# Kernel optimization log

Hardware: AMD Instinct MI355X
Metric: run time of the kernel (lower is better)

Reference implementation:

```python
import jax, jax.numpy as jnp
import numpy as np

N_NODES = 50000
N_EDGES = 400000
HEADS = 3
CH = 128
NEG_SLOPE = 0.2
EPS = 1e-16


def setup_inputs() -> dict:
    key = jax.random.key(0)
    ks = jax.random.split(key, 10)
    return {
        "x": jax.random.normal(ks[0], (N_NODES, 9), jnp.float32),
        "emb_w": jax.random.normal(ks[1], (9, 128), jnp.float32) * 0.1,
        "emb_b": jax.random.normal(ks[2], (128,), jnp.float32) * 0.1,
        "gat_w": jax.random.normal(ks[3], (128, HEADS * CH), jnp.float32) * 0.05,
        "att_src": jax.random.normal(ks[4], (HEADS, CH), jnp.float32) * 0.1,
        "att_dst": jax.random.normal(ks[5], (HEADS, CH), jnp.float32) * 0.1,
        "gat_bias": jax.random.normal(ks[6], (CH,), jnp.float32) * 0.1,
        "out_w": jax.random.normal(ks[7], (128, 4), jnp.float32) * 0.1,
        "out_b": jax.random.normal(ks[8], (4,), jnp.float32) * 0.1,
        "edge_index": jax.random.randint(ks[9], (2, N_EDGES), 0, N_NODES, jnp.int64 if jax.config.jax_enable_x64 else jnp.int32),
    }


def reference(x, emb_w, emb_b, gat_w, att_src, att_dst, gat_bias, out_w, out_b, edge_index):
    n = x.shape[0]
    h = x @ emb_w + emb_b                                   # [N,128]
    # add self loops (PyG GATConv default)
    loops = jnp.arange(n, dtype=edge_index.dtype)
    src = jnp.concatenate([edge_index[0], loops])
    dst = jnp.concatenate([edge_index[1], loops])
    xh = (h @ gat_w).reshape(n, HEADS, CH)                  # [N,H,C]
    a_src = jnp.einsum('nhc,hc->nh', xh, att_src)           # [N,H]
    a_dst = jnp.einsum('nhc,hc->nh', xh, att_dst)           # [N,H]
    e = a_src[src] + a_dst[dst]                             # [E,H]
    e = jax.nn.leaky_relu(e, NEG_SLOPE)
    # segment softmax over destination node
    e_max = jax.ops.segment_max(e, dst, num_segments=n)
    e = jnp.exp(e - e_max[dst])
    denom = jax.ops.segment_sum(e, dst, num_segments=n)
    alpha = e / (denom[dst] + EPS)                          # [E,H]
    msg = xh[src] * alpha[:, :, None]                       # [E,H,C]
    agg = jax.ops.segment_sum(msg, dst, num_segments=n)     # [N,H,C]
    out = agg.mean(axis=1) + gat_bias                       # concat=False -> head mean
    x_new = out + h                                         # residual
    return x_new @ out_w + out_b                            # [N,4]
```

## Files before the change

### kernel.cpp

```cpp
#include <hip/hip_runtime.h>
#include <hip/hip_bf16.h>
#include <cstdint>

#define NEG 0.2f
#define SBS 256
#define SCAN2_T 1024
#define PADK 56

typedef __attribute__((ext_vector_type(8))) short bf16x8;
typedef __attribute__((ext_vector_type(4))) float f32x4;

__device__ __forceinline__ float bf2f(unsigned short u){
  return __uint_as_float(((unsigned)u)<<16);
}
__device__ __forceinline__ unsigned short f2bf(float f){
  __hip_bfloat16 b = __float2bfloat16(f);
  return *reinterpret_cast<unsigned short*>(&b);
}

__global__ __launch_bounds__(256)
void prep_kernel(const float* __restrict__ gat_w, const float* __restrict__ att_src,
                 const float* __restrict__ att_dst, float* __restrict__ w_att_s,
                 float* __restrict__ w_att_d, unsigned short* __restrict__ Bt2)
{
  if (blockIdx.x < 192){
    int wave = threadIdx.x >> 6, lane = threadIdx.x & 63;
    int o = blockIdx.x*4 + wave;
    if (o >= 768) return;
    int isD = (o >= 384);
    int t = isD ? (o - 384) : o;
    int h = t >> 7, k = t & 127;
    const float* att = isD ? att_dst : att_src;
    int c = 2*lane;
    float g0 = gat_w[(size_t)k*384 + h*128 + c];
    float g1 = gat_w[(size_t)k*384 + h*128 + c + 1];
    float dot = g0*att[h*128+c] + g1*att[h*128+c+1];
    #pragma unroll
    for (int off=32; off; off>>=1) dot += __shfl_down(dot, off);
    if (lane==0){
      if (isD) w_att_d[t] = dot; else w_att_s[t] = dot;
    }
  } else {
    int i = (blockIdx.x-192)*256 + threadIdx.x;
    if (i >= 12*128*32) return;
    int ks  = i >> 12;
    int rem = i & 4095;
    int col = rem >> 5;
    int kk  = rem & 31;
    int t = ks*32 + kk;
    int h = t >> 7, k = t & 127;
    Bt2[i] = f2bf(gat_w[(size_t)k*384 + h*128 + col] * (1.f/3.f));
  }
}

__global__ __launch_bounds__(256)
void embed_kernel(const float* __restrict__ x, const float* __restrict__ emb_w,
                  const float* __restrict__ emb_b, const float* __restrict__ w_att_s,
                  const float* __restrict__ w_att_d,
                  unsigned short* __restrict__ h_bf, float* __restrict__ a_s,
                  float* __restrict__ a_d, int nN)
{
  int n = blockIdx.x*256 + threadIdx.x;
  if (n >= nN) return;

  float xv[9];
  #pragma unroll
  for (int k=0;k<9;k++) xv[k] = x[(size_t)n*9 + k];

  float s0=0.f,s1=0.f,s2=0.f, d0=0.f,d1=0.f,d2=0.f;
  unsigned short* hrow = h_bf + (size_t)n*128;

  #pragma unroll 4
  for (int c0=0; c0<128; c0+=8){
    unsigned short pk[8];
    #pragma unroll
    for (int j=0;j<8;j++){
      int c = c0 + j;
      float acc = emb_b[c];
      #pragma unroll
      for (int k=0;k<9;k++) acc += xv[k]*emb_w[k*128+c];
      pk[j] = f2bf(acc);
      s0 += acc*w_att_s[c]; s1 += acc*w_att_s[128+c]; s2 += acc*w_att_s[256+c];
      d0 += acc*w_att_d[c]; d1 += acc*w_att_d[128+c]; d2 += acc*w_att_d[256+c];
    }
    *(int4*)(hrow + c0) = *(int4*)pk;
  }
  a_s[(size_t)n*3+0]=s0; a_s[(size_t)n*3+1]=s1; a_s[(size_t)n*3+2]=s2;
  a_d[(size_t)n*3+0]=d0; a_d[(size_t)n*3+1]=d1; a_d[(size_t)n*3+2]=d2;
}

__global__ __launch_bounds__(256)
void deg_kernel(const int* __restrict__ ei, int* __restrict__ deg, int nE)
{
  int e = blockIdx.x*256 + threadIdx.x;
  if (e < nE) atomicAdd(&deg[ei[nE + e]], 1);
}

__global__ __launch_bounds__(SBS)
void blocksum_kernel(const int* __restrict__ deg, int* __restrict__ bsum, int nN)
{
  int i = blockIdx.x*SBS + threadIdx.x;
  int v = (i < nN) ? deg[i] : 0;
  #pragma unroll
  for (int off=32; off; off>>=1) v += __shfl_down(v, off);
  __shared__ int ws[SBS/64];
  if ((threadIdx.x&63)==0) ws[threadIdx.x>>6] = v;
  __syncthreads();
  if (threadIdx.x==0){
    int s=0;
    #pragma unroll
    for (int i2=0;i2<SBS/64;i2++) s += ws[i2];
    bsum[blockIdx.x]=s;
  }
}

__global__ __launch_bounds__(SCAN2_T)
void scansum_kernel(const int* __restrict__ bsum, int* __restrict__ boff, int nB)
{
  __shared__ int s[SCAN2_T];
  int t = threadIdx.x;
  int v = (t < nB) ? bsum[t] : 0;
  s[t] = v;
  __syncthreads();
  for (int off=1; off<SCAN2_T; off<<=1){
    int add = (t >= off) ? s[t-off] : 0;
    __syncthreads();
    s[t] += add;
    __syncthreads();
  }
  if (t < nB) boff[t] = (t==0) ? 0 : s[t-1];
}

__global__ __launch_bounds__(SBS)
void blockscan_kernel(const int* __restrict__ deg, const int* __restrict__ boff,
                      int* __restrict__ rowptr, int* __restrict__ cursor, int nN)
{
  __shared__ int s[SBS];
  int t = threadIdx.x;
  int i = blockIdx.x*SBS + t;
  int v = (i < nN) ? deg[i] : 0;
  s[t] = v;
  __syncthreads();
  for (int off=1; off<SBS; off<<=1){
    int add = (t >= off) ? s[t-off] : 0;
    __syncthreads();
    s[t] += add;
    __syncthreads();
  }
  int excl = boff[blockIdx.x] + ((t==0) ? 0 : s[t-1]);
  if (i < nN){ rowptr[i] = excl; cursor[i] = excl; }
  if (i == nN-1) rowptr[nN] = excl + v;
}

__global__ __launch_bounds__(256)
void scatter_kernel(const int* __restrict__ ei, int* __restrict__ cursor,
                    int* __restrict__ csr, int nE)
{
  int e = blockIdx.x*256 + threadIdx.x;
  if (e < nE){
    int s = ei[e], d = ei[nE + e];
    int pos = atomicAdd(&cursor[d], 1);
    csr[pos] = s;
  }
}

__global__ __launch_bounds__(256)
void gather_kernel(const int* __restrict__ rowptr, const int* __restrict__ csr,
                   const float* __restrict__ a_s, const float* __restrict__ a_d,
                   const unsigned short* __restrict__ h_bf,
                   unsigned short* __restrict__ hagg, int nN)
{
  int wave = threadIdx.x >> 6, lane = threadIdx.x & 63;
  int n = blockIdx.x*4 + wave;
  if (n >= nN) return;

  int ro  = rowptr[n];
  int deg = rowptr[n+1] - ro;
  int degT = deg + 1;
  float ad0 = a_d[(size_t)n*3+0], ad1 = a_d[(size_t)n*3+1], ad2 = a_d[(size_t)n*3+2];

  float d0=0.f, d1=0.f, d2=0.f;
  float acc00=0.f, acc01=0.f, acc10=0.f, acc11=0.f, acc20=0.f, acc21=0.f;

  for (int base=0; base<degT; base+=64){
    int i = base + lane;
    int sReg = n; float p0=0.f, p1=0.f, p2=0.f;
    if (i < degT){
      int s = (i < deg) ? csr[ro+i] : n;
      sReg = s;
      float e0 = a_s[(size_t)s*3+0] + ad0; e0 = e0>0.f ? e0 : NEG*e0;
      float e1 = a_s[(size_t)s*3+1] + ad1; e1 = e1>0.f ? e1 : NEG*e1;
      float e2 = a_s[(size_t)s*3+2] + ad2; e2 = e2>0.f ? e2 : NEG*e2;
      p0 = __expf(e0); p1 = __expf(e1); p2 = __expf(e2);
      d0 += p0; d1 += p1; d2 += p2;
    }
    int cnt = min(64, degT - base);
    for (int j=0;j<cnt;j++){
      int   s  = __shfl(sReg, j);
      float A0 = __shfl(p0, j);
      float A1 = __shfl(p1, j);
      float A2 = __shfl(p2, j);
      ushort2 hv = *(const ushort2*)(h_bf + (size_t)s*128 + 2*lane);
      float f0 = bf2f(hv.x), f1 = bf2f(hv.y);
      acc00 += A0*f0; acc01 += A0*f1;
      acc10 += A1*f0; acc11 += A1*f1;
      acc20 += A2*f0; acc21 += A2*f1;
    }
  }
  #pragma unroll
  for (int off=1; off<64; off<<=1){
    d0 += __shfl_xor(d0, off);
    d1 += __shfl_xor(d1, off);
    d2 += __shfl_xor(d2, off);
  }
  float w0 = 1.f/(d0+1e-16f);
  float w1 = 1.f/(d1+1e-16f);
  float w2 = 1.f/(d2+1e-16f);

  size_t base = (size_t)n*384 + 2*lane;
  ushort2 o0 = {f2bf(acc00*w0), f2bf(acc01*w0)};
  ushort2 o1 = {f2bf(acc10*w1), f2bf(acc11*w1)};
  ushort2 o2 = {f2bf(acc20*w2), f2bf(acc21*w2)};
  *(ushort2*)(hagg + base      ) = o0;
  *(ushort2*)(hagg + base + 128) = o1;
  *(ushort2*)(hagg + base + 256) = o2;
}

__global__ __launch_bounds__(256)
void gemm2_kernel(const unsigned short* __restrict__ hagg,
                  const unsigned short* __restrict__ Bt2,
                  const unsigned short* __restrict__ h_bf,
                  const float* __restrict__ gat_bias,
                  const float* __restrict__ out_w, const float* __restrict__ out_b,
                  float* __restrict__ out, int nN)
{
  __shared__ __align__(16) unsigned short Bs[2][128*PADK];
  int tid  = threadIdx.x;
  int wave = tid >> 6, lane = tid & 63;
  int cl = lane & 15, kg = lane >> 4;
  int r0 = blockIdx.x*64 + wave*16;
  int rowA = min(r0 + cl, nN-1);
  const unsigned short* aBase = hagg + (size_t)rowA*384 + kg*8;

  int scol = tid >> 1, shalf = tid & 1;
  int dstI = scol*(PADK/8) + shalf*2;

  {
    const int4* src = (const int4*)Bt2;
    int4 t0 = src[2*tid], t1 = src[2*tid+1];
    ((int4*)Bs[0])[dstI]   = t0;
    ((int4*)Bs[0])[dstI+1] = t1;
  }
  f32x4 acc[8];
  #pragma unroll
  for (int f=0;f<8;f++) acc[f] = (f32x4){0.f,0.f,0.f,0.f};
  bf16x8 aCur = *(const bf16x8*)(aBase);
  __syncthreads();

  #pragma unroll
  for (int ks=0; ks<12; ks++){
    int4 t0, t1; bf16x8 aNext;
    if (ks < 11){
      const int4* src = (const int4*)(Bt2 + (size_t)(ks+1)*4096);
      t0 = src[2*tid]; t1 = src[2*tid+1];
      aNext = *(const bf16x8*)(aBase + (ks+1)*32);
    }
    const unsigned short* bs = Bs[ks & 1];
    #pragma unroll
    for (int f=0;f<8;f++){
      bf16x8 b = *(const bf16x8*)(bs + (f*16 + cl)*PADK + kg*8);
      acc[f] = __builtin_amdgcn_mfma_f32_16x16x32_bf16(aCur, b, acc[f], 0, 0, 0);
    }
    if (ks < 11){
      int4* dst = (int4*)Bs[(ks+1) & 1];
      dst[dstI]   = t0;
      dst[dstI+1] = t1;
      aCur = aNext;
    }
    __syncthreads();
  }

  float p[4][4];
  #pragma unroll
  for (int r=0;r<4;r++)
    #pragma unroll
    for (int j=0;j<4;j++) p[r][j]=0.f;

  #pragma unroll
  for (int f=0;f<8;f++){
    int col = f*16 + cl;
    float bias = gat_bias[col];
    float w0=out_w[col*4+0], w1=out_w[col*4+1], w2=out_w[col*4+2], w3=out_w[col*4+3];
    #pragma unroll
    for (int r=0;r<4;r++){
      int row = r0 + kg*4 + r;
      float hres = (row < nN) ? bf2f(h_bf[(size_t)row*128 + col]) : 0.f;
      float xn = acc[f][r] + bias + hres;
      p[r][0] += xn*w0; p[r][1] += xn*w1; p[r][2] += xn*w2; p[r][3] += xn*w3;
    }
  }
  #pragma unroll
  for (int off=1; off<16; off<<=1){
    #pragma unroll
    for (int r=0;r<4;r++)
      #pragma unroll
      for (int j=0;j<4;j++) p[r][j] += __shfl_xor(p[r][j], off);
  }
  if (cl == 0){
    #pragma unroll
    for (int r=0;r<4;r++){
      int row = r0 + kg*4 + r;
      if (row < nN){
        float4 o = {p[r][0]+out_b[0], p[r][1]+out_b[1], p[r][2]+out_b[2], p[r][3]+out_b[3]};
        *(float4*)(out + (size_t)row*4) = o;
      }
    }
  }
}

extern "C" void kernel_launch(void* const* d_in, const int* in_sizes, int n_in,
                              void* d_out, int out_size, void* d_ws, size_t ws_size,
                              hipStream_t stream) {
  const float* x       = (const float*)d_in[0];
  const float* emb_w   = (const float*)d_in[1];
  const float* emb_b   = (const float*)d_in[2];
  const float* gat_w   = (const float*)d_in[3];
  const float* att_src = (const float*)d_in[4];
  const float* att_dst = (const float*)d_in[5];
  const float* gat_bias= (const float*)d_in[6];
  const float* out_w   = (const float*)d_in[7];
  const float* out_b   = (const float*)d_in[8];
  const int*   ei      = (const int*)d_in[9];
  float* out = (float*)d_out;

  int nN = in_sizes[0]/9;
  int nE = in_sizes[9]/2;
  int nB = (nN + SBS - 1) / SBS;

  char* p = (char*)d_ws;
  auto alloc = [&](size_t bytes)->char*{
    char* r = p; p += (bytes + 255) & ~(size_t)255; return r;
  };
  unsigned short* h_bf   = (unsigned short*)alloc((size_t)nN*128*2);
  float*          a_s    = (float*)         alloc((size_t)nN*3*4);
  float*          a_d    = (float*)         alloc((size_t)nN*3*4);
  float*          w_att_s= (float*)         alloc(384*4);
  float*          w_att_d= (float*)         alloc(384*4);
  unsigned short* Bt2    = (unsigned short*)alloc((size_t)12*128*32*2);
  int*            deg    = (int*)           alloc((size_t)nN*4);
  int*            rowptr = (int*)           alloc(((size_t)nN+1)*4);
  int*            cursor = (int*)           alloc((size_t)nN*4);
  int*            csr    = (int*)           alloc((size_t)nE*4);
  int*            bsum   = (int*)           alloc((size_t)nB*4);
  int*            boff   = (int*)           alloc((size_t)nB*4);
  unsigned short* hagg   = (unsigned short*)alloc((size_t)nN*384*2);

  hipMemsetAsync(deg, 0, (size_t)nN*4, stream);

  prep_kernel<<<384, 256, 0, stream>>>(gat_w, att_src, att_dst, w_att_s, w_att_d, Bt2);

  embed_kernel<<<(nN+255)/256, 256, 0, stream>>>(
      x, emb_w, emb_b, w_att_s, w_att_d, h_bf, a_s, a_d, nN);

  deg_kernel<<<(nE+255)/256, 256, 0, stream>>>(ei, deg, nE);
  blocksum_kernel<<<nB, SBS, 0, stream>>>(deg, bsum, nN);
  scansum_kernel<<<1, SCAN2_T, 0, stream>>>(bsum, boff, nB);
  blockscan_kernel<<<nB, SBS, 0, stream>>>(deg, boff, rowptr, cursor, nN);
  scatter_kernel<<<(nE+255)/256, 256, 0, stream>>>(ei, cursor, csr, nE);

  gather_kernel<<<(nN+3)/4, 256, 0, stream>>>(
      rowptr, csr, a_s, a_d, h_bf, hagg, nN);

  gemm2_kernel<<<(nN+63)/64, 256, 0, stream>>>(
      hagg, Bt2, h_bf, gat_bias, out_w, out_b, out, nN);
}
```

Baseline: 226.6 us.

## Process four destination nodes per wave with 16-lane groups and 16-byte gathers

The gather kernel now splits each wave into four 16-lane groups, one destination node per group. Each lane loads 8 bf16 features at once with a 16-byte vector load and handles two neighbours per inner iteration. Before, one wave per node did 4-byte loads and looped serially over every neighbour. The change is meant to cut idle lanes and per-edge shuffle overhead when average degree is about 9, and to widen memory transactions. In exchange it uses more registers (24 accumulators) and sees divergence when the nodes sharing a wave have different degrees.

```diff
diff --git a/kernel.cpp b/kernel.cpp
--- a/kernel.cpp
+++ b/kernel.cpp
@@ -8,6 +8,7 @@
 #define PADK 56
 
 typedef __attribute__((ext_vector_type(8))) short bf16x8;
+typedef __attribute__((ext_vector_type(8))) unsigned short ushort8;
 typedef __attribute__((ext_vector_type(4))) float f32x4;
 
 __device__ __forceinline__ float bf2f(unsigned short u){
@@ -171,22 +172,31 @@
                    unsigned short* __restrict__ hagg, int nN)
 {
   int wave = threadIdx.x >> 6, lane = threadIdx.x & 63;
-  int n = blockIdx.x*4 + wave;
-  if (n >= nN) return;
-
-  int ro  = rowptr[n];
-  int deg = rowptr[n+1] - ro;
-  int degT = deg + 1;
-  float ad0 = a_d[(size_t)n*3+0], ad1 = a_d[(size_t)n*3+1], ad2 = a_d[(size_t)n*3+2];
-
+  int g   = lane >> 4;
+  int lin = lane & 15;
+  int gb  = lane & 48;
+  int n = blockIdx.x*16 + wave*4 + g;
+  int valid = (n < nN);
+  int nc = valid ? n : (nN-1);
+
+  int ro  = rowptr[nc];
+  int deg = rowptr[nc+1] - ro;
+  int degT = valid ? (deg + 1) : 0;
+
+  float ad0 = a_d[(size_t)nc*3+0], ad1 = a_d[(size_t)nc*3+1], ad2 = a_d[(size_t)nc*3+2];
+
+  float acc0[8], acc1[8], acc2[8];
+  #pragma unroll
+  for (int c=0;c<8;c++){ acc0[c]=0.f; acc1[c]=0.f; acc2[c]=0.f; }
   float d0=0.f, d1=0.f, d2=0.f;
-  float acc00=0.f, acc01=0.f, acc10=0.f, acc11=0.f, acc20=0.f, acc21=0.f;
-
-  for (int base=0; base<degT; base+=64){
-    int i = base + lane;
-    int sReg = n; float p0=0.f, p1=0.f, p2=0.f;
+
+  const unsigned short* hb8 = h_bf + 8*lin;
+
+  for (int base=0; base<degT; base+=16){
+    int i = base + lin;
+    int sReg = nc; float p0=0.f, p1=0.f, p2=0.f;
     if (i < degT){
-      int s = (i < deg) ? csr[ro+i] : n;
+      int s = (i < deg) ? csr[ro+i] : nc;
       sReg = s;
       float e0 = a_s[(size_t)s*3+0] + ad0; e0 = e0>0.f ? e0 : NEG*e0;
       float e1 = a_s[(size_t)s*3+1] + ad1; e1 = e1>0.f ? e1 : NEG*e1;
@@ -194,36 +204,59 @@
       p0 = __expf(e0); p1 = __expf(e1); p2 = __expf(e2);
       d0 += p0; d1 += p1; d2 += p2;
     }
-    int cnt = min(64, degT - base);
-    for (int j=0;j<cnt;j++){
-      int   s  = __shfl(sReg, j);
-      float A0 = __shfl(p0, j);
-      float A1 = __shfl(p1, j);
-      float A2 = __shfl(p2, j);
-      ushort2 hv = *(const ushort2*)(h_bf + (size_t)s*128 + 2*lane);
-      float f0 = bf2f(hv.x), f1 = bf2f(hv.y);
-      acc00 += A0*f0; acc01 += A0*f1;
-      acc10 += A1*f0; acc11 += A1*f1;
-      acc20 += A2*f0; acc21 += A2*f1;
-    }
-  }
-  #pragma unroll
-  for (int off=1; off<64; off<<=1){
+    int cnt = min(16, degT - base);
+    int j = 0;
+    for (; j+1 < cnt; j += 2){
+      int   sA = __shfl(sReg, gb+j);
+      int   sB = __shfl(sReg, gb+j+1);
+      float A0 = __shfl(p0, gb+j),   A1 = __shfl(p1, gb+j),   A2 = __shfl(p2, gb+j);
+      float B0 = __shfl(p0, gb+j+1), B1 = __shfl(p1, gb+j+1), B2 = __shfl(p2, gb+j+1);
+      ushort8 ha = *(const ushort8*)(hb8 + (size_t)sA*128);
+      ushort8 hb = *(const ushort8*)(hb8 + (size_t)sB*128);
+      #pragma unroll
+      for (int c=0;c<8;c++){
+        float fa = bf2f(ha[c]);
+        float fb = bf2f(hb[c]);
+        acc0[c] += A0*fa + B0*fb;
+        acc1[c] += A1*fa + B1*fb;
+        acc2[c] += A2*fa + B2*fb;
+      }
+    }
+    if (j < cnt){
+      int   sA = __shfl(sReg, gb+j);
+      float A0 = __shfl(p0, gb+j), A1 = __shfl(p1, gb+j), A2 = __shfl(p2, gb+j);
+      ushort8 ha = *(const ushort8*)(hb8 + (size_t)sA*128);
+      #pragma unroll
+      for (int c=0;c<8;c++){
+        float fa = bf2f(ha[c]);
+        acc0[c] += A0*fa; acc1[c] += A1*fa; acc2[c] += A2*fa;
+      }
+    }
+  }
+
+  #pragma unroll
+  for (int off=1; off<16; off<<=1){
     d0 += __shfl_xor(d0, off);
     d1 += __shfl_xor(d1, off);
     d2 += __shfl_xor(d2, off);
   }
-  float w0 = 1.f/(d0+1e-16f);
-  float w1 = 1.f/(d1+1e-16f);
-  float w2 = 1.f/(d2+1e-16f);
-
-  size_t base = (size_t)n*384 + 2*lane;
-  ushort2 o0 = {f2bf(acc00*w0), f2bf(acc01*w0)};
-  ushort2 o1 = {f2bf(acc10*w1), f2bf(acc11*w1)};
-  ushort2 o2 = {f2bf(acc20*w2), f2bf(acc21*w2)};
-  *(ushort2*)(hagg + base      ) = o0;
-  *(ushort2*)(hagg + base + 128) = o1;
-  *(ushort2*)(hagg + base + 256) = o2;
+
+  if (valid){
+    float w0 = 1.f/(d0+1e-16f);
+    float w1 = 1.f/(d1+1e-16f);
+    float w2 = 1.f/(d2+1e-16f);
+    unsigned short o0[8], o1[8], o2[8];
+    #pragma unroll
+    for (int c=0;c<8;c++){
+      o0[c] = f2bf(acc0[c]*w0);
+      o1[c] = f2bf(acc1[c]*w1);
+      o2[c] = f2bf(acc2[c]*w2);
+    }
+    size_t bidx = (size_t)n*384 + 8*lin;
+    *(int4*)(hagg + bidx      ) = *(int4*)o0;
+    *(int4*)(hagg + bidx + 128) = *(int4*)o1;
+    *(int4*)(hagg + bidx + 256) = *(int4*)o2;
+  }
 }
 
 __global__ __launch_bounds__(256)
@@ -368,7 +401,7 @@
   blockscan_kernel<<<nB, SBS, 0, stream>>>(deg, boff, rowptr, cursor, nN);
   scatter_kernel<<<(nE+255)/256, 256, 0, stream>>>(ei, cursor, csr, nE);
 
-  gather_kernel<<<(nN+3)/4, 256, 0, stream>>>(
+  gather_kernel<<<(nN+15)/16, 256, 0, stream>>>(
       rowptr, csr, a_s, a_d, h_bf, hagg, nN);
 
   gemm2_kernel<<<(nN+63)/64, 256, 0, stream>>>(
```

After: 210.5 us. 1.08x faster.
